# Kernel tuning notes

Measured on AMD Instinct MI355X. Metric: run time of the kernel, lower is better.

Reference implementation:

```python
import jax, jax.numpy as jnp
from jax import lax
import numpy as np

T, D, DFF, E, K = 1024, 2048, 1024, 16, 6


def setup_inputs() -> dict:
    key = jax.random.key(0)
    ks = jax.random.split(key, 9)
    x = jax.random.normal(ks[0], (T, D), dtype=jnp.float32)
    selected_experts = jax.random.randint(ks[1], (T, K), 0, E, dtype=jnp.int64)
    rw = jax.random.uniform(ks[2], (T, K), dtype=jnp.float32)
    routing_weights = rw / jnp.sum(rw, axis=-1, keepdims=True)  # normalized top-k weights
    # Expert weights: w0 (gate), w1 (up): [E, DFF, D]; w2 (down): [E, D, DFF]
    w0 = jax.random.normal(ks[3], (E, DFF, D), dtype=jnp.float32) * (D ** -0.5)
    w1 = jax.random.normal(ks[4], (E, DFF, D), dtype=jnp.float32) * (D ** -0.5)
    w2 = jax.random.normal(ks[5], (E, D, DFF), dtype=jnp.float32) * (DFF ** -0.5)
    # Per-expert dequant scales (s0/s1/s2 in the fused kernel)
    s0 = jax.random.uniform(ks[6], (E,), dtype=jnp.float32, minval=0.5, maxval=1.5)
    s1 = jax.random.uniform(ks[7], (E,), dtype=jnp.float32, minval=0.5, maxval=1.5)
    s2 = jax.random.uniform(ks[8], (E,), dtype=jnp.float32, minval=0.5, maxval=1.5)
    return {"x": x, "w0": w0, "w1": w1, "w2": w2, "s0": s0, "s1": s1, "s2": s2,
            "selected_experts": selected_experts, "routing_weights": routing_weights}


def reference(x, w0, w1, w2, s0, s1, s2, selected_experts, routing_weights):
    num_experts = w0.shape[0]
    # combine weights per (token, expert): sum of routing weights over top-k slots
    onehot = jax.nn.one_hot(selected_experts, num_experts, dtype=x.dtype)  # [T,K,E]
    cw = jnp.einsum('tke,tk->et', onehot, routing_weights)                 # [E,T]

    def body(acc, inp):
        w0e, w1e, w2e, s0e, s1e, s2e, cwe = inp
        g = (x @ w0e.T) * s0e                 # [T,DFF] gate proj (dequant scale)
        u = (x @ w1e.T) * s1e                 # [T,DFF] up proj
        h = jax.nn.silu(g) * u                # SwiGLU
        y = (h @ w2e.T) * s2e                 # [T,D] down proj
        return acc + cwe[:, None] * y, None

    out, _ = lax.scan(body, jnp.zeros_like(x), (w0, w1, w2, s0, s1, s2, cw))
    return out
```

## Files before the change

### kernel.cpp

```cpp
#include <hip/hip_runtime.h>
#include <hip/hip_bf16.h>
#include <stdint.h>

#define T_TOK 1024
#define D_DIM 2048
#define DFF   1024
#define NE    16
#define TOPK  6
#define KD    (NE * DFF)

typedef float f32x4 __attribute__((ext_vector_type(4)));
typedef __bf16 bf16x8 __attribute__((ext_vector_type(8)));
typedef unsigned short u16x8 __attribute__((ext_vector_type(8)));

__device__ __forceinline__ unsigned short f2bf(float f) {
    union { float f; unsigned int u; } v; v.f = f;
    unsigned int x = v.u;
    unsigned int r = x + 0x7FFFu + ((x >> 16) & 1u);
    return (unsigned short)(r >> 16);
}


__global__ void cvt_f32_bf16(const float* __restrict__ src,
                             unsigned short* __restrict__ dst, int n4) {
    int i = blockIdx.x * blockDim.x + threadIdx.x;
    int stride = gridDim.x * blockDim.x;
    for (; i < n4; i += stride) {
        float4 v = ((const float4*)src)[i];
        ushort4 o;
        o.x = f2bf(v.x); o.y = f2bf(v.y); o.z = f2bf(v.z); o.w = f2bf(v.w);
        ((ushort4*)dst)[i] = o;
    }
}

__global__ void cvt_w2_transpose(const float* __restrict__ w2,
                                 unsigned short* __restrict__ dst, int n4) {
    int i = blockIdx.x * blockDim.x + threadIdx.x;
    int stride = gridDim.x * blockDim.x;
    const int F4 = DFF / 4;
    for (; i < n4; i += stride) {
        int f4 = i % F4;
        int rest = i / F4;
        int d = rest % D_DIM;
        int e = rest / D_DIM;
        float4 v = ((const float4*)w2)[(size_t)(e * D_DIM + d) * F4 + f4];
        ushort4 o;
        o.x = f2bf(v.x); o.y = f2bf(v.y); o.z = f2bf(v.z); o.w = f2bf(v.w);
        ((ushort4*)dst)[(size_t)d * (KD / 4) + e * F4 + f4] = o;
    }
}

__global__ void cw_scatter(const int* __restrict__ sel,
                           const float* __restrict__ rw,
                           float* __restrict__ cw) {
    int i = blockIdx.x * blockDim.x + threadIdx.x;
    if (i < T_TOK * TOPK) {
        int t = i / TOPK;
        int e = sel[i];
        atomicAdd(&cw[e * T_TOK + t], rw[i]);
    }
}

__global__ __launch_bounds__(256, 2)
void gemm1_kernel(const unsigned short* __restrict__ xb,
                  const unsigned short* __restrict__ wb0,
                  const unsigned short* __restrict__ wb1,
                  const float* __restrict__ cw,
                  const float* __restrict__ s0,
                  const float* __restrict__ s1,
                  const float* __restrict__ s2,
                  unsigned short* __restrict__ hs)
{
    const int tf = blockIdx.x, tt = blockIdx.y, e = blockIdx.z;
    const int tid = threadIdx.x;
    const int lane = tid & 63, wid = tid >> 6;
    const int wm = wid >> 1, wn = wid & 1;
    const int quad = lane >> 4, l16 = lane & 15;

    __shared__ alignas(16) unsigned short sA [128 * 64];
    __shared__ alignas(16) unsigned short sB0[128 * 64];
    __shared__ alignas(16) unsigned short sB1[128 * 64];
    __shared__ float cws[128];

    if (tid < 128) cws[tid] = cw[e * T_TOK + tt * 128 + tid];

    const unsigned short* a_base  = xb  + (size_t)(tt * 128) * D_DIM;
    const unsigned short* b0_base = wb0 + ((size_t)e * DFF + tf * 128) * D_DIM;
    const unsigned short* b1_base = wb1 + ((size_t)e * DFF + tf * 128) * D_DIM;

    f32x4 accG[4][4], accU[4][4];
    const f32x4 zz = {0.f, 0.f, 0.f, 0.f};
#pragma unroll
    for (int mi = 0; mi < 4; ++mi)
#pragma unroll
        for (int ni = 0; ni < 4; ++ni) { accG[mi][ni] = zz; accU[mi][ni] = zz; }

    for (int k0 = 0; k0 < D_DIM; k0 += 64) {
        u16x8 rA[4], rB0[4], rB1[4];
#pragma unroll
        for (int it = 0; it < 4; ++it) {
            int c = it * 256 + tid;
            int row = c >> 3, col = c & 7;
            rA [it] = *(const u16x8*)(a_base  + (size_t)row * D_DIM + k0 + col * 8);
            rB0[it] = *(const u16x8*)(b0_base + (size_t)row * D_DIM + k0 + col * 8);
            rB1[it] = *(const u16x8*)(b1_base + (size_t)row * D_DIM + k0 + col * 8);
        }
        __syncthreads();
#pragma unroll
        for (int it = 0; it < 4; ++it) {
            int c = it * 256 + tid;
            int row = c >> 3, col = c & 7;
            int cs = col ^ (row & 7);
            *(u16x8*)(sA  + row * 64 + cs * 8) = rA [it];
            *(u16x8*)(sB0 + row * 64 + cs * 8) = rB0[it];
            *(u16x8*)(sB1 + row * 64 + cs * 8) = rB1[it];
        }
        __syncthreads();
#pragma unroll
        for (int kk = 0; kk < 2; ++kk) {
            bf16x8 af[4], b0f[4], b1f[4];
#pragma unroll
            for (int mi = 0; mi < 4; ++mi) {
                int row = wm * 64 + mi * 16 + l16;
                int cch = (kk * 4 + quad) ^ (row & 7);
                af[mi] = __builtin_bit_cast(bf16x8,
                         *(const u16x8*)(sA + row * 64 + cch * 8));
            }
#pragma unroll
            for (int ni = 0; ni < 4; ++ni) {
                int row = wn * 64 + ni * 16 + l16;
                int cch = (kk * 4 + quad) ^ (row & 7);
                b0f[ni] = __builtin_bit_cast(bf16x8,
                          *(const u16x8*)(sB0 + row * 64 + cch * 8));
                b1f[ni] = __builtin_bit_cast(bf16x8,
                          *(const u16x8*)(sB1 + row * 64 + cch * 8));
            }
#pragma unroll
            for (int mi = 0; mi < 4; ++mi)
#pragma unroll
                for (int ni = 0; ni < 4; ++ni) {
                    accG[mi][ni] = __builtin_amdgcn_mfma_f32_16x16x32_bf16(
                        af[mi], b0f[ni], accG[mi][ni], 0, 0, 0);
                    accU[mi][ni] = __builtin_amdgcn_mfma_f32_16x16x32_bf16(
                        af[mi], b1f[ni], accU[mi][ni], 0, 0, 0);
                }
        }
    }

    const float s0e = s0[e], s1e = s1[e], s2e = s2[e];
#pragma unroll
    for (int mi = 0; mi < 4; ++mi) {
#pragma unroll
        for (int reg = 0; reg < 4; ++reg) {
            int tl = wm * 64 + mi * 16 + quad * 4 + reg;
            float cwt = cws[tl] * s2e;
            size_t t = (size_t)(tt * 128 + tl);
#pragma unroll
            for (int ni = 0; ni < 4; ++ni) {
                float g = accG[mi][ni][reg] * s0e;
                float u = accU[mi][ni][reg] * s1e;
                float h = g / (1.f + __expf(-g)) * u;
                float val = h * cwt;
                int fc = tf * 128 + wn * 64 + ni * 16 + l16;
                hs[t * KD + e * DFF + fc] = f2bf(val);
            }
        }
    }
}

__global__ __launch_bounds__(256, 2)
void gemm2_kernel(const unsigned short* __restrict__ hsrc,
                  const unsigned short* __restrict__ wb2t,
                  float* __restrict__ part)
{
    const int td = blockIdx.x, tt = blockIdx.y, sp = blockIdx.z;
    const int tid = threadIdx.x;
    const int lane = tid & 63, wid = tid >> 6;
    const int wm = wid >> 1, wn = wid & 1;
    const int quad = lane >> 4, l16 = lane & 15;

    __shared__ alignas(16) unsigned short sA[128 * 64];
    __shared__ alignas(16) unsigned short sB[128 * 64];

    const unsigned short* a_base = hsrc + (size_t)(tt * 128) * KD;
    const unsigned short* b_base = wb2t + (size_t)(td * 128) * KD;

    f32x4 acc[4][4];
    const f32x4 zz = {0.f, 0.f, 0.f, 0.f};
#pragma unroll
    for (int mi = 0; mi < 4; ++mi)
#pragma unroll
        for (int ni = 0; ni < 4; ++ni) acc[mi][ni] = zz;

    const int kbeg = sp * (KD / 4);
    const int kend = kbeg + (KD / 4);
    for (int k0 = kbeg; k0 < kend; k0 += 64) {
        u16x8 rA[4], rB[4];
#pragma unroll
        for (int it = 0; it < 4; ++it) {
            int c = it * 256 + tid;
            int row = c >> 3, col = c & 7;
            rA[it] = *(const u16x8*)(a_base + (size_t)row * KD + k0 + col * 8);
            rB[it] = *(const u16x8*)(b_base + (size_t)row * KD + k0 + col * 8);
        }
        __syncthreads();
#pragma unroll
        for (int it = 0; it < 4; ++it) {
            int c = it * 256 + tid;
            int row = c >> 3, col = c & 7;
            int cs = col ^ (row & 7);
            *(u16x8*)(sA + row * 64 + cs * 8) = rA[it];
            *(u16x8*)(sB + row * 64 + cs * 8) = rB[it];
        }
        __syncthreads();
#pragma unroll
        for (int kk = 0; kk < 2; ++kk) {
            bf16x8 af[4], bf[4];
#pragma unroll
            for (int mi = 0; mi < 4; ++mi) {
                int row = wm * 64 + mi * 16 + l16;
                int cch = (kk * 4 + quad) ^ (row & 7);
                af[mi] = __builtin_bit_cast(bf16x8,
                         *(const u16x8*)(sA + row * 64 + cch * 8));
            }
#pragma unroll
            for (int ni = 0; ni < 4; ++ni) {
                int row = wn * 64 + ni * 16 + l16;
                int cch = (kk * 4 + quad) ^ (row & 7);
                bf[ni] = __builtin_bit_cast(bf16x8,
                         *(const u16x8*)(sB + row * 64 + cch * 8));
            }
#pragma unroll
            for (int mi = 0; mi < 4; ++mi)
#pragma unroll
                for (int ni = 0; ni < 4; ++ni)
                    acc[mi][ni] = __builtin_amdgcn_mfma_f32_16x16x32_bf16(
                        af[mi], bf[ni], acc[mi][ni], 0, 0, 0);
        }
    }

    float* pout = part + (size_t)sp * T_TOK * D_DIM;
#pragma unroll
    for (int mi = 0; mi < 4; ++mi)
#pragma unroll
        for (int reg = 0; reg < 4; ++reg) {
            int t = tt * 128 + wm * 64 + mi * 16 + quad * 4 + reg;
            size_t rowoff = (size_t)t * D_DIM;
#pragma unroll
            for (int ni = 0; ni < 4; ++ni) {
                int d = td * 128 + wn * 64 + ni * 16 + l16;
                pout[rowoff + d] = acc[mi][ni][reg];
            }
        }
}

__global__ void reduce4(const float* __restrict__ part, float* __restrict__ out, int n4) {
    int i = blockIdx.x * blockDim.x + threadIdx.x;
    int stride = gridDim.x * blockDim.x;
    const float4* p0 = (const float4*)(part);
    const float4* p1 = (const float4*)(part + (size_t)T_TOK * D_DIM);
    const float4* p2 = (const float4*)(part + (size_t)2 * T_TOK * D_DIM);
    const float4* p3 = (const float4*)(part + (size_t)3 * T_TOK * D_DIM);
    for (; i < n4; i += stride) {
        float4 a = p0[i], b = p1[i], c = p2[i], d = p3[i];
        float4 o;
        o.x = a.x + b.x + c.x + d.x;
        o.y = a.y + b.y + c.y + d.y;
        o.z = a.z + b.z + c.z + d.z;
        o.w = a.w + b.w + c.w + d.w;
        ((float4*)out)[i] = o;
    }
}


extern "C" void kernel_launch(void* const* d_in, const int* in_sizes, int n_in,
                              void* d_out, int out_size, void* d_ws, size_t ws_size,
                              hipStream_t stream) {
    const float* x  = (const float*)d_in[0];
    const float* w0 = (const float*)d_in[1];
    const float* w1 = (const float*)d_in[2];
    const float* w2 = (const float*)d_in[3];
    const float* s0 = (const float*)d_in[4];
    const float* s1 = (const float*)d_in[5];
    const float* s2 = (const float*)d_in[6];
    const int*   sel = (const int*)d_in[7];
    const float* rw = (const float*)d_in[8];
    float* out = (float*)d_out;

    char* ws = (char*)d_ws;
    constexpr size_t WB0_OFF  = 0;
    constexpr size_t WB1_OFF  = 67108864ull;
    constexpr size_t HS_OFF   = 134217728ull;
    constexpr size_t XB_OFF   = 167772160ull;
    constexpr size_t CW_OFF   = 171966464ull;
    unsigned short* wb0  = (unsigned short*)(ws + WB0_OFF);
    unsigned short* wb1  = (unsigned short*)(ws + WB1_OFF);
    unsigned short* wb2t = (unsigned short*)(ws + WB0_OFF);
    float*          partb= (float*)        (ws + WB1_OFF);
    unsigned short* hsb  = (unsigned short*)(ws + HS_OFF);
    unsigned short* xb   = (unsigned short*)(ws + XB_OFF);
    float*          cw   = (float*)        (ws + CW_OFF);

    hipMemsetAsync(cw, 0, NE * T_TOK * sizeof(float), stream);
    cw_scatter<<<(T_TOK * TOPK + 255) / 256, 256, 0, stream>>>(sel, rw, cw);

    cvt_f32_bf16<<<2048, 256, 0, stream>>>(x, xb, T_TOK * D_DIM / 4);
    cvt_f32_bf16<<<4096, 256, 0, stream>>>(w0, wb0, NE * DFF * D_DIM / 4);
    cvt_f32_bf16<<<4096, 256, 0, stream>>>(w1, wb1, NE * DFF * D_DIM / 4);

    gemm1_kernel<<<dim3(DFF / 128, T_TOK / 128, NE), 256, 0, stream>>>(
        xb, wb0, wb1, cw, s0, s1, s2, hsb);

    cvt_w2_transpose<<<4096, 256, 0, stream>>>(w2, wb2t, NE * D_DIM * DFF / 4);

    gemm2_kernel<<<dim3(D_DIM / 128, T_TOK / 128, 4), 256, 0, stream>>>(
        hsb, wb2t, partb);

    reduce4<<<2048, 256, 0, stream>>>(partb, out, T_TOK * D_DIM / 4);
}
```

Measured before the change: 633.0 us.

## Route tokens sparsely per expert and fuse fp32-to-bf16 conversion into GEMM loads

Builds per-expert token lists from the combine weights, so each expert's GEMMs only process routed tokens (gathered rows) instead of all tokens with zero weights. Weight and activation conversion to bf16 is folded into the GEMM global loads, removing the separate conversion and transpose kernels and their workspace traffic. The down projection now scatters results into the output with atomicAdd per expert, replacing the split-K partials and reduce kernel. In exchange, the output is nondeterministic because of atomics, the GEMMs read fp32 weights directly (double the bytes per tile load), and rounding changes slightly (round-half-up without tie-to-even).

```diff
diff --git a/kernel.cpp b/kernel.cpp
--- a/kernel.cpp
+++ b/kernel.cpp
@@ -7,7 +7,6 @@
 #define DFF   1024
 #define NE    16
 #define TOPK  6
-#define KD    (NE * DFF)
 
 typedef float f32x4 __attribute__((ext_vector_type(4)));
 typedef __bf16 bf16x8 __attribute__((ext_vector_type(8)));
@@ -20,35 +19,20 @@
     return (unsigned short)(r >> 16);
 }
 
-
-__global__ void cvt_f32_bf16(const float* __restrict__ src,
-                             unsigned short* __restrict__ dst, int n4) {
-    int i = blockIdx.x * blockDim.x + threadIdx.x;
-    int stride = gridDim.x * blockDim.x;
-    for (; i < n4; i += stride) {
-        float4 v = ((const float4*)src)[i];
-        ushort4 o;
-        o.x = f2bf(v.x); o.y = f2bf(v.y); o.z = f2bf(v.z); o.w = f2bf(v.w);
-        ((ushort4*)dst)[i] = o;
-    }
-}
-
-__global__ void cvt_w2_transpose(const float* __restrict__ w2,
-                                 unsigned short* __restrict__ dst, int n4) {
-    int i = blockIdx.x * blockDim.x + threadIdx.x;
-    int stride = gridDim.x * blockDim.x;
-    const int F4 = DFF / 4;
-    for (; i < n4; i += stride) {
-        int f4 = i % F4;
-        int rest = i / F4;
-        int d = rest % D_DIM;
-        int e = rest / D_DIM;
-        float4 v = ((const float4*)w2)[(size_t)(e * D_DIM + d) * F4 + f4];
-        ushort4 o;
-        o.x = f2bf(v.x); o.y = f2bf(v.y); o.z = f2bf(v.z); o.w = f2bf(v.w);
-        ((ushort4*)dst)[(size_t)d * (KD / 4) + e * F4 + f4] = o;
-    }
-}
+__device__ __forceinline__ unsigned int pack_bf2(float x, float y) {
+    unsigned int a = __builtin_bit_cast(unsigned int, x) + 0x8000u;
+    unsigned int b = __builtin_bit_cast(unsigned int, y) + 0x8000u;
+    return __builtin_amdgcn_perm(b, a, 0x07060302);
+}
+__device__ __forceinline__ u16x8 cvt8(float4 p, float4 q) {
+    union { u16x8 v; unsigned int w[4]; } u;
+    u.w[0] = pack_bf2(p.x, p.y);
+    u.w[1] = pack_bf2(p.z, p.w);
+    u.w[2] = pack_bf2(q.x, q.y);
+    u.w[3] = pack_bf2(q.z, q.w);
+    return u.v;
+}
+
 
 __global__ void cw_scatter(const int* __restrict__ sel,
                            const float* __restrict__ rw,
@@ -61,17 +45,37 @@
     }
 }
 
+__global__ void build_lists(const float* __restrict__ cw,
+                            int* __restrict__ list,
+                            int* __restrict__ count) {
+    int i = blockIdx.x * blockDim.x + threadIdx.x;
+    if (i < NE * T_TOK) {
+        int e = i >> 10;
+        float c = cw[i];
+        if (c != 0.f) {
+            int p = atomicAdd(&count[e], 1);
+            list[(e << 10) + p] = i & 1023;
+        }
+    }
+}
+
 __global__ __launch_bounds__(256, 2)
-void gemm1_kernel(const unsigned short* __restrict__ xb,
-                  const unsigned short* __restrict__ wb0,
-                  const unsigned short* __restrict__ wb1,
+void gemm1_kernel(const float* __restrict__ xf,
+                  const float* __restrict__ w0,
+                  const float* __restrict__ w1,
                   const float* __restrict__ cw,
+                  const int* __restrict__ list,
+                  const int* __restrict__ count,
                   const float* __restrict__ s0,
                   const float* __restrict__ s1,
                   const float* __restrict__ s2,
-                  unsigned short* __restrict__ hs)
+                  unsigned short* __restrict__ hc)
 {
-    const int tf = blockIdx.x, tt = blockIdx.y, e = blockIdx.z;
+    const int tf = blockIdx.x, tile = blockIdx.y, e = blockIdx.z;
+    const int n_e = count[e];
+    const int base = tile * 128;
+    if (base >= n_e) return;
+
     const int tid = threadIdx.x;
     const int lane = tid & 63, wid = tid >> 6;
     const int wm = wid >> 1, wn = wid & 1;
@@ -80,13 +84,24 @@
     __shared__ alignas(16) unsigned short sA [128 * 64];
     __shared__ alignas(16) unsigned short sB0[128 * 64];
     __shared__ alignas(16) unsigned short sB1[128 * 64];
+    __shared__ int   slist[128];
     __shared__ float cws[128];
 
-    if (tid < 128) cws[tid] = cw[e * T_TOK + tt * 128 + tid];
-
-    const unsigned short* a_base  = xb  + (size_t)(tt * 128) * D_DIM;
-    const unsigned short* b0_base = wb0 + ((size_t)e * DFF + tf * 128) * D_DIM;
-    const unsigned short* b1_base = wb1 + ((size_t)e * DFF + tf * 128) * D_DIM;
+    if (tid < 128) {
+        int idx = base + tid;
+        int cl = idx < n_e ? idx : (n_e - 1);
+        int tok = list[(e << 10) + cl];
+        slist[tid] = tok;
+        cws[tid] = (idx < n_e) ? cw[e * T_TOK + tok] : 0.f;
+    }
+    __syncthreads();
+
+    int rowtok[4];
+#pragma unroll
+    for (int it = 0; it < 4; ++it) rowtok[it] = slist[it * 32 + (tid >> 3)];
+
+    const float* b0_base = w0 + ((size_t)e * DFF + tf * 128) * D_DIM;
+    const float* b1_base = w1 + ((size_t)e * DFF + tf * 128) * D_DIM;
 
     f32x4 accG[4][4], accU[4][4];
     const f32x4 zz = {0.f, 0.f, 0.f, 0.f};
@@ -101,9 +116,15 @@
         for (int it = 0; it < 4; ++it) {
             int c = it * 256 + tid;
             int row = c >> 3, col = c & 7;
-            rA [it] = *(const u16x8*)(a_base  + (size_t)row * D_DIM + k0 + col * 8);
-            rB0[it] = *(const u16x8*)(b0_base + (size_t)row * D_DIM + k0 + col * 8);
-            rB1[it] = *(const u16x8*)(b1_base + (size_t)row * D_DIM + k0 + col * 8);
+            const float* ap = xf + (size_t)rowtok[it] * D_DIM + k0 + col * 8;
+            float4 a0 = *(const float4*)ap, a1 = *(const float4*)(ap + 4);
+            const float* bp0 = b0_base + (size_t)row * D_DIM + k0 + col * 8;
+            float4 b00 = *(const float4*)bp0, b01 = *(const float4*)(bp0 + 4);
+            const float* bp1 = b1_base + (size_t)row * D_DIM + k0 + col * 8;
+            float4 b10 = *(const float4*)bp1, b11 = *(const float4*)(bp1 + 4);
+            rA [it] = cvt8(a0, a1);
+            rB0[it] = cvt8(b00, b01);
+            rB1[it] = cvt8(b10, b11);
         }
         __syncthreads();
 #pragma unroll
@@ -154,26 +175,31 @@
         for (int reg = 0; reg < 4; ++reg) {
             int tl = wm * 64 + mi * 16 + quad * 4 + reg;
             float cwt = cws[tl] * s2e;
-            size_t t = (size_t)(tt * 128 + tl);
+            size_t slot = (size_t)((e << 10) + base + tl);
 #pragma unroll
             for (int ni = 0; ni < 4; ++ni) {
                 float g = accG[mi][ni][reg] * s0e;
                 float u = accU[mi][ni][reg] * s1e;
                 float h = g / (1.f + __expf(-g)) * u;
-                float val = h * cwt;
                 int fc = tf * 128 + wn * 64 + ni * 16 + l16;
-                hs[t * KD + e * DFF + fc] = f2bf(val);
+                hc[slot * DFF + fc] = f2bf(h * cwt);
             }
         }
     }
 }
 
 __global__ __launch_bounds__(256, 2)
-void gemm2_kernel(const unsigned short* __restrict__ hsrc,
-                  const unsigned short* __restrict__ wb2t,
-                  float* __restrict__ part)
+void gemm2_kernel(const unsigned short* __restrict__ hc,
+                  const float* __restrict__ w2,
+                  const int* __restrict__ list,
+                  const int* __restrict__ count,
+                  float* __restrict__ out)
 {
-    const int td = blockIdx.x, tt = blockIdx.y, sp = blockIdx.z;
+    const int td = blockIdx.x, tile = blockIdx.y, e = blockIdx.z;
+    const int n_e = count[e];
+    const int base = tile * 128;
+    if (base >= n_e) return;
+
     const int tid = threadIdx.x;
     const int lane = tid & 63, wid = tid >> 6;
     const int wm = wid >> 1, wn = wid & 1;
@@ -181,9 +207,17 @@
 
     __shared__ alignas(16) unsigned short sA[128 * 64];
     __shared__ alignas(16) unsigned short sB[128 * 64];
-
-    const unsigned short* a_base = hsrc + (size_t)(tt * 128) * KD;
-    const unsigned short* b_base = wb2t + (size_t)(td * 128) * KD;
+    __shared__ int slist[128];
+
+    if (tid < 128) {
+        int idx = base + tid;
+        int cl = idx < n_e ? idx : (n_e - 1);
+        slist[tid] = list[(e << 10) + cl];
+    }
+    __syncthreads();
+
+    const unsigned short* a_base = hc + (size_t)((e << 10) + base) * DFF;
+    const float* b_base = w2 + ((size_t)e * D_DIM + td * 128) * DFF;
 
     f32x4 acc[4][4];
     const f32x4 zz = {0.f, 0.f, 0.f, 0.f};
@@ -192,16 +226,16 @@
 #pragma unroll
         for (int ni = 0; ni < 4; ++ni) acc[mi][ni] = zz;
 
-    const int kbeg = sp * (KD / 4);
-    const int kend = kbeg + (KD / 4);
-    for (int k0 = kbeg; k0 < kend; k0 += 64) {
+    for (int k0 = 0; k0 < DFF; k0 += 64) {
         u16x8 rA[4], rB[4];
 #pragma unroll
         for (int it = 0; it < 4; ++it) {
             int c = it * 256 + tid;
             int row = c >> 3, col = c & 7;
-            rA[it] = *(const u16x8*)(a_base + (size_t)row * KD + k0 + col * 8);
-            rB[it] = *(const u16x8*)(b_base + (size_t)row * KD + k0 + col * 8);
+            rA[it] = *(const u16x8*)(a_base + (size_t)row * DFF + k0 + col * 8);
+            const float* bp = b_base + (size_t)row * DFF + k0 + col * 8;
+            float4 b0 = *(const float4*)bp, b1 = *(const float4*)(bp + 4);
+            rB[it] = cvt8(b0, b1);
         }
         __syncthreads();
 #pragma unroll
@@ -215,7 +249,7 @@
         __syncthreads();
 #pragma unroll
         for (int kk = 0; kk < 2; ++kk) {
-            bf16x8 af[4], bf[4];
+            bf16x8 af[4], bfr[4];
 #pragma unroll
             for (int mi = 0; mi < 4; ++mi) {
                 int row = wm * 64 + mi * 16 + l16;
@@ -227,49 +261,33 @@
             for (int ni = 0; ni < 4; ++ni) {
                 int row = wn * 64 + ni * 16 + l16;
                 int cch = (kk * 4 + quad) ^ (row & 7);
-                bf[ni] = __builtin_bit_cast(bf16x8,
-                         *(const u16x8*)(sB + row * 64 + cch * 8));
+                bfr[ni] = __builtin_bit_cast(bf16x8,
+                          *(const u16x8*)(sB + row * 64 + cch * 8));
             }
 #pragma unroll
             for (int mi = 0; mi < 4; ++mi)
 #pragma unroll
                 for (int ni = 0; ni < 4; ++ni)
                     acc[mi][ni] = __builtin_amdgcn_mfma_f32_16x16x32_bf16(
-                        af[mi], bf[ni], acc[mi][ni], 0, 0, 0);
-        }
-    }
-
-    float* pout = part + (size_t)sp * T_TOK * D_DIM;
+                        af[mi], bfr[ni], acc[mi][ni], 0, 0, 0);
+        }
+    }
+
 #pragma unroll
     for (int mi = 0; mi < 4; ++mi)
 #pragma unroll
         for (int reg = 0; reg < 4; ++reg) {
-            int t = tt * 128 + wm * 64 + mi * 16 + quad * 4 + reg;
-            size_t rowoff = (size_t)t * D_DIM;
-#pragma unroll
-            for (int ni = 0; ni < 4; ++ni) {
-                int d = td * 128 + wn * 64 + ni * 16 + l16;
-                pout[rowoff + d] = acc[mi][ni][reg];
-            }
-        }
-}
-
-__global__ void reduce4(const float* __restrict__ part, float* __restrict__ out, int n4) {
-    int i = blockIdx.x * blockDim.x + threadIdx.x;
-    int stride = gridDim.x * blockDim.x;
-    const float4* p0 = (const float4*)(part);
-    const float4* p1 = (const float4*)(part + (size_t)T_TOK * D_DIM);
-    const float4* p2 = (const float4*)(part + (size_t)2 * T_TOK * D_DIM);
-    const float4* p3 = (const float4*)(part + (size_t)3 * T_TOK * D_DIM);
-    for (; i < n4; i += stride) {
-        float4 a = p0[i], b = p1[i], c = p2[i], d = p3[i];
-        float4 o;
-        o.x = a.x + b.x + c.x + d.x;
-        o.y = a.y + b.y + c.y + d.y;
-        o.z = a.z + b.z + c.z + d.z;
-        o.w = a.w + b.w + c.w + d.w;
-        ((float4*)out)[i] = o;
-    }
+            int tl = wm * 64 + mi * 16 + quad * 4 + reg;
+            if (base + tl < n_e) {
+                int tok = slist[tl];
+                float* orow = out + (size_t)tok * D_DIM;
+#pragma unroll
+                for (int ni = 0; ni < 4; ++ni) {
+                    int d = td * 128 + wn * 64 + ni * 16 + l16;
+                    atomicAdd(orow + d, acc[mi][ni][reg]);
+                }
+            }
+        }
 }
 
 
@@ -288,33 +306,24 @@
     float* out = (float*)d_out;
 
     char* ws = (char*)d_ws;
-    constexpr size_t WB0_OFF  = 0;
-    constexpr size_t WB1_OFF  = 67108864ull;
-    constexpr size_t HS_OFF   = 134217728ull;
-    constexpr size_t XB_OFF   = 167772160ull;
-    constexpr size_t CW_OFF   = 171966464ull;
-    unsigned short* wb0  = (unsigned short*)(ws + WB0_OFF);
-    unsigned short* wb1  = (unsigned short*)(ws + WB1_OFF);
-    unsigned short* wb2t = (unsigned short*)(ws + WB0_OFF);
-    float*          partb= (float*)        (ws + WB1_OFF);
-    unsigned short* hsb  = (unsigned short*)(ws + HS_OFF);
-    unsigned short* xb   = (unsigned short*)(ws + XB_OFF);
-    float*          cw   = (float*)        (ws + CW_OFF);
-
-    hipMemsetAsync(cw, 0, NE * T_TOK * sizeof(float), stream);
+    constexpr size_t HC_OFF    = 0;
+    constexpr size_t LIST_OFF  = 33554432ull;
+    constexpr size_t CW_OFF    = LIST_OFF + 65536ull;
+    constexpr size_t COUNT_OFF = CW_OFF + 65536ull;
+    unsigned short* hc    = (unsigned short*)(ws + HC_OFF);
+    int*            list  = (int*)           (ws + LIST_OFF);
+    float*          cw    = (float*)         (ws + CW_OFF);
+    int*            count = (int*)           (ws + COUNT_OFF);
+
+    hipMemsetAsync(cw, 0, 65536 + 256, stream);
     cw_scatter<<<(T_TOK * TOPK + 255) / 256, 256, 0, stream>>>(sel, rw, cw);
-
-    cvt_f32_bf16<<<2048, 256, 0, stream>>>(x, xb, T_TOK * D_DIM / 4);
-    cvt_f32_bf16<<<4096, 256, 0, stream>>>(w0, wb0, NE * DFF * D_DIM / 4);
-    cvt_f32_bf16<<<4096, 256, 0, stream>>>(w1, wb1, NE * DFF * D_DIM / 4);
+    build_lists<<<(NE * T_TOK + 255) / 256, 256, 0, stream>>>(cw, list, count);
+
+    hipMemsetAsync(out, 0, (size_t)T_TOK * D_DIM * sizeof(float), stream);
 
     gemm1_kernel<<<dim3(DFF / 128, T_TOK / 128, NE), 256, 0, stream>>>(
-        xb, wb0, wb1, cw, s0, s1, s2, hsb);
-
-    cvt_w2_transpose<<<4096, 256, 0, stream>>>(w2, wb2t, NE * D_DIM * DFF / 4);
-
-    gemm2_kernel<<<dim3(D_DIM / 128, T_TOK / 128, 4), 256, 0, stream>>>(
-        hsb, wb2t, partb);
-
-    reduce4<<<2048, 256, 0, stream>>>(partb, out, T_TOK * D_DIM / 4);
-}
+        x, w0, w1, cw, list, count, s0, s1, s2, hc);
+
+    gemm2_kernel<<<dim3(D_DIM / 128, T_TOK / 128, NE), 256, 0, stream>>>(
+        hc, w2, list, count, out);
+}
```

After: 558.6 us. 1.13x faster.
